# Performance work log

Hardware: AMD Instinct MI355X
Metric: run time of the kernel (lower is better)

The kernel has to match this reference:

```python
import jax, jax.numpy as jnp
import numpy as np
from jax import lax

B, T, D, H = 256, 1024, 64, 100


def setup_inputs() -> dict:
    key = jax.random.key(0)
    ks = jax.random.split(key, 8)
    s = 1.0 / np.sqrt(H)  # PyTorch LSTM/Linear init scale
    x = jax.random.normal(ks[0], (B, T, D), dtype=jnp.float32)
    h0 = jnp.zeros((1, B, H), dtype=jnp.float32)
    c0 = jnp.zeros((1, B, H), dtype=jnp.float32)
    # PyTorch gate order: i, f, g, o stacked along first dim (4H)
    W_ih = jax.random.uniform(ks[1], (4 * H, D), jnp.float32, -s, s)
    W_hh = jax.random.uniform(ks[2], (4 * H, H), jnp.float32, -s, s)
    b_ih = jax.random.uniform(ks[3], (4 * H,), jnp.float32, -s, s)
    b_hh = jax.random.uniform(ks[4], (4 * H,), jnp.float32, -s, s)
    W_fc = jax.random.uniform(ks[5], (1, H), jnp.float32, -s, s)
    b_fc = jax.random.uniform(ks[6], (1,), jnp.float32, -s, s)
    return {"x": x, "h0": h0, "c0": c0, "W_ih": W_ih, "W_hh": W_hh,
            "b_ih": b_ih, "b_hh": b_hh, "W_fc": W_fc, "b_fc": b_fc}


def reference(x, h0, c0, W_ih, W_hh, b_ih, b_hh, W_fc, b_fc):
    # Precompute input contribution to all gates in one big GEMM: [B,T,4H]
    xg = jnp.einsum('btd,gd->btg', x, W_ih) + (b_ih + b_hh)

    def step(carry, xt):  # xt: [B,4H]
        h, c = carry
        gates = xt + h @ W_hh.T
        i, f, g, o = jnp.split(gates, 4, axis=-1)
        i = jax.nn.sigmoid(i)
        f = jax.nn.sigmoid(f)
        g = jnp.tanh(g)
        o = jax.nn.sigmoid(o)
        c = f * c + i * g
        h = o * jnp.tanh(c)
        return (h, c), None

    (h_T, _), _ = lax.scan(step, (h0[0], c0[0]), jnp.swapaxes(xg, 0, 1))
    # dropout is identity in eval mode; fc head on final hidden state
    out = h_T @ W_fc.T + b_fc  # [B, 1]
    return out
```

## Files before the change

### kernel.cpp

```cpp
#include <hip/hip_runtime.h>
#include <math.h>

#define BATCH 256
#define TSTEPS 1024
#define DIN 64
#define HID 100
#define GATES 400
#define BLOCK 512
#define XT 32

__global__ __launch_bounds__(BLOCK, 1)
void lstm_fused_kernel(const float* __restrict__ x, const float* __restrict__ h0,
                       const float* __restrict__ c0, const float* __restrict__ W_ih,
                       const float* __restrict__ W_hh, const float* __restrict__ b_ih,
                       const float* __restrict__ b_hh, const float* __restrict__ W_fc,
                       const float* __restrict__ b_fc, float* __restrict__ out)
{
    __shared__ __align__(16) float h_buf[2][104];
    __shared__ __align__(16) float x_tile[XT * DIN];
    __shared__ float red[128];

    const int tid = threadIdx.x;
    const int b = blockIdx.x;
    const int q = tid & 3;
    const int n = tid >> 2;
    const int g = q * HID + n;
    const int gl = (tid < GATES) ? g : 0;

    float wih[DIN];
    float whh[HID];
    {
        const float4* wi4 = reinterpret_cast<const float4*>(W_ih + gl * DIN);
        #pragma unroll
        for (int k = 0; k < DIN / 4; ++k) {
            float4 v = wi4[k];
            wih[4*k+0] = v.x; wih[4*k+1] = v.y; wih[4*k+2] = v.z; wih[4*k+3] = v.w;
        }
        const float4* wh4 = reinterpret_cast<const float4*>(W_hh + gl * HID);
        #pragma unroll
        for (int k = 0; k < HID / 4; ++k) {
            float4 v = wh4[k];
            whh[4*k+0] = v.x; whh[4*k+1] = v.y; whh[4*k+2] = v.z; whh[4*k+3] = v.w;
        }
    }
    #pragma unroll
    for (int k = 0; k < DIN; ++k) asm volatile("" : "+v"(wih[k]));
    #pragma unroll
    for (int k = 0; k < HID; ++k) asm volatile("" : "+v"(whh[k]));

    const float bias = b_ih[gl] + b_hh[gl];

    if (tid < HID) h_buf[0][tid] = h0[b * HID + tid];
    float c = 0.f;
    if (q == 0 && n < HID) c = c0[b * HID + n];
    __syncthreads();

    for (int tt = 0; tt < TSTEPS; tt += XT) {
        {
            const float4* xs = reinterpret_cast<const float4*>(
                x + (size_t)b * TSTEPS * DIN + (size_t)tt * DIN);
            reinterpret_cast<float4*>(x_tile)[tid] = xs[tid];
        }
        __syncthreads();

        #pragma unroll 2
        for (int t2 = 0; t2 < XT; ++t2) {
            const int t = tt + t2;
            const int cur = t & 1, nxt = cur ^ 1;

            float a0 = 0.f, a1 = 0.f, a2 = 0.f, a3 = 0.f;
            const float4* h4 = reinterpret_cast<const float4*>(h_buf[cur]);
            #pragma unroll
            for (int k = 0; k < HID / 4; ++k) {
                float4 hv = h4[k];
                a0 += hv.x * whh[4*k+0];
                a1 += hv.y * whh[4*k+1];
                a2 += hv.z * whh[4*k+2];
                a3 += hv.w * whh[4*k+3];
            }
            const float4* x4 = reinterpret_cast<const float4*>(&x_tile[t2 * DIN]);
            #pragma unroll
            for (int k = 0; k < DIN / 4; ++k) {
                float4 xv = x4[k];
                a0 += xv.x * wih[4*k+0];
                a1 += xv.y * wih[4*k+1];
                a2 += xv.z * wih[4*k+2];
                a3 += xv.w * wih[4*k+3];
            }
            float z = ((a0 + a1) + (a2 + a3)) + bias;

            float zq = (q == 2) ? 2.f * z : z;
            float e = __expf(-zq);
            float s = 1.f / (1.f + e);
            float a = (q == 2) ? (2.f * s - 1.f) : s;

            float fv = __shfl_down(a, 1);
            float gv = __shfl_down(a, 2);
            float ov = __shfl_down(a, 3);
            if (q == 0 && n < HID) {
                c = fv * c + a * gv;
                float e2 = __expf(-2.f * c);
                float th = 2.f / (1.f + e2) - 1.f;
                h_buf[nxt][n] = ov * th;
            }
            __syncthreads();
        }
    }

    if (tid < HID) red[tid] = h_buf[0][tid] * W_fc[tid];
    __syncthreads();
    if (tid == 0) {
        float s = 0.f;
        #pragma unroll 4
        for (int i = 0; i < HID; ++i) s += red[i];
        out[b] = s + b_fc[0];
    }
}

extern "C" void kernel_launch(void* const* d_in, const int* in_sizes, int n_in,
                              void* d_out, int out_size, void* d_ws, size_t ws_size,
                              hipStream_t stream) {
    const float* x    = (const float*)d_in[0];
    const float* h0   = (const float*)d_in[1];
    const float* c0   = (const float*)d_in[2];
    const float* W_ih = (const float*)d_in[3];
    const float* W_hh = (const float*)d_in[4];
    const float* b_ih = (const float*)d_in[5];
    const float* b_hh = (const float*)d_in[6];
    const float* W_fc = (const float*)d_in[7];
    const float* b_fc = (const float*)d_in[8];
    float* out = (float*)d_out;

    lstm_fused_kernel<<<dim3(BATCH), dim3(BLOCK), 0, stream>>>(
        x, h0, c0, W_ih, W_hh, b_ih, b_hh, W_fc, b_fc, out);
}
```

Baseline: 1.060 ms.

## Split each gate's dot product across two threads and use fast reciprocal activations

Result: faster. 927.2 us (-12.5%).

```diff
diff --git a/kernel.cpp b/kernel.cpp
--- a/kernel.cpp
+++ b/kernel.cpp
@@ -5,9 +5,9 @@
 #define TSTEPS 1024
 #define DIN 64
 #define HID 100
-#define GATES 400
-#define BLOCK 512
+#define BLOCK 832
 #define XT 32
+
 
 __global__ __launch_bounds__(BLOCK, 1)
 void lstm_fused_kernel(const float* __restrict__ x, const float* __restrict__ h0,
@@ -22,41 +22,41 @@
 
     const int tid = threadIdx.x;
     const int b = blockIdx.x;
-    const int q = tid & 3;
-    const int n = tid >> 2;
-    const int g = q * HID + n;
-    const int gl = (tid < GATES) ? g : 0;
+    const int p  = tid & 1;
+    const int gq = tid >> 1;
+    const int q  = gq & 3;
+    const int n  = gq >> 2;
+    const int nl = (n < HID) ? n : (HID - 1);
+    const int gl = q * HID + nl;
 
-    float wih[DIN];
-    float whh[HID];
-    {
-        const float4* wi4 = reinterpret_cast<const float4*>(W_ih + gl * DIN);
-        #pragma unroll
-        for (int k = 0; k < DIN / 4; ++k) {
-            float4 v = wi4[k];
-            wih[4*k+0] = v.x; wih[4*k+1] = v.y; wih[4*k+2] = v.z; wih[4*k+3] = v.w;
-        }
-        const float4* wh4 = reinterpret_cast<const float4*>(W_hh + gl * HID);
-        #pragma unroll
-        for (int k = 0; k < HID / 4; ++k) {
-            float4 v = wh4[k];
-            whh[4*k+0] = v.x; whh[4*k+1] = v.y; whh[4*k+2] = v.z; whh[4*k+3] = v.w;
-        }
-    }
+    const int cb  = p * 48;
+    const int cb2 = p * 32;
+
+    float whh[52];
     #pragma unroll
-    for (int k = 0; k < DIN; ++k) asm volatile("" : "+v"(wih[k]));
+    for (int j = 0; j < 52; ++j) whh[j] = W_hh[gl * HID + cb + j];
+    if (p) { whh[0] = 0.f; whh[1] = 0.f; whh[2] = 0.f; whh[3] = 0.f; }
+    float wih[32];
     #pragma unroll
-    for (int k = 0; k < HID; ++k) asm volatile("" : "+v"(whh[k]));
+    for (int j = 0; j < 32; ++j) wih[j] = W_ih[gl * DIN + cb2 + j];
+    #pragma unroll
+    for (int j = 0; j < 52; ++j) asm volatile("" : "+v"(whh[j]));
+    #pragma unroll
+    for (int j = 0; j < 32; ++j) asm volatile("" : "+v"(wih[j]));
 
-    const float bias = b_ih[gl] + b_hh[gl];
+    const float bias = (p == 0) ? (b_ih[gl] + b_hh[gl]) : 0.f;
+
+    const float mQ = (q == 2) ?  2.f : -1.f;
+    const float aQ = (q == 2) ?  1.f :  0.f;
+    const float bQ = (q == 2) ? -2.f :  1.f;
 
     if (tid < HID) h_buf[0][tid] = h0[b * HID + tid];
     float c = 0.f;
-    if (q == 0 && n < HID) c = c0[b * HID + n];
+    if ((tid & 7) == 0) c = c0[b * HID + nl];
     __syncthreads();
 
     for (int tt = 0; tt < TSTEPS; tt += XT) {
-        {
+        if (tid < 512) {
             const float4* xs = reinterpret_cast<const float4*>(
                 x + (size_t)b * TSTEPS * DIN + (size_t)tt * DIN);
             reinterpret_cast<float4*>(x_tile)[tid] = xs[tid];
@@ -65,42 +65,41 @@
 
         #pragma unroll 2
         for (int t2 = 0; t2 < XT; ++t2) {
-            const int t = tt + t2;
-            const int cur = t & 1, nxt = cur ^ 1;
+            const int cur = (tt + t2) & 1, nxt = cur ^ 1;
 
             float a0 = 0.f, a1 = 0.f, a2 = 0.f, a3 = 0.f;
-            const float4* h4 = reinterpret_cast<const float4*>(h_buf[cur]);
+            const float4* h4 = reinterpret_cast<const float4*>(&h_buf[cur][cb]);
             #pragma unroll
-            for (int k = 0; k < HID / 4; ++k) {
+            for (int k = 0; k < 13; ++k) {
                 float4 hv = h4[k];
                 a0 += hv.x * whh[4*k+0];
                 a1 += hv.y * whh[4*k+1];
                 a2 += hv.z * whh[4*k+2];
                 a3 += hv.w * whh[4*k+3];
             }
-            const float4* x4 = reinterpret_cast<const float4*>(&x_tile[t2 * DIN]);
+            const float4* x4 = reinterpret_cast<const float4*>(&x_tile[t2 * DIN + cb2]);
             #pragma unroll
-            for (int k = 0; k < DIN / 4; ++k) {
+            for (int k = 0; k < 8; ++k) {
                 float4 xv = x4[k];
                 a0 += xv.x * wih[4*k+0];
                 a1 += xv.y * wih[4*k+1];
                 a2 += xv.z * wih[4*k+2];
                 a3 += xv.w * wih[4*k+3];
             }
-            float z = ((a0 + a1) + (a2 + a3)) + bias;
+            float sum = ((a0 + a1) + (a2 + a3)) + bias;
+            float z = sum + __shfl_xor(sum, 1);
 
-            float zq = (q == 2) ? 2.f * z : z;
-            float e = __expf(-zq);
-            float s = 1.f / (1.f + e);
-            float a = (q == 2) ? (2.f * s - 1.f) : s;
+            float e = __expf(mQ * z);
+            float s = __builtin_amdgcn_rcpf(1.f + e);
+            float a = fmaf(bQ, s, aQ);
 
-            float fv = __shfl_down(a, 1);
-            float gv = __shfl_down(a, 2);
-            float ov = __shfl_down(a, 3);
-            if (q == 0 && n < HID) {
-                c = fv * c + a * gv;
-                float e2 = __expf(-2.f * c);
-                float th = 2.f / (1.f + e2) - 1.f;
+            float fv = __shfl_down(a, 2);
+            float gv = __shfl_down(a, 4);
+            float ov = __shfl_down(a, 6);
+            if ((tid & 7) == 0) {
+                c = fmaf(fv, c, a * gv);
+                float e2 = __expf(c + c);
+                float th = fmaf(-2.f, __builtin_amdgcn_rcpf(1.f + e2), 1.f);
                 h_buf[nxt][n] = ov * th;
             }
             __syncthreads();
@@ -110,10 +109,10 @@
     if (tid < HID) red[tid] = h_buf[0][tid] * W_fc[tid];
     __syncthreads();
     if (tid == 0) {
-        float s = 0.f;
+        float sfc = 0.f;
         #pragma unroll 4
-        for (int i = 0; i < HID; ++i) s += red[i];
-        out[b] = s + b_fc[0];
+        for (int i = 0; i < HID; ++i) sfc += red[i];
+        out[b] = sfc + b_fc[0];
     }
 }
 
```
